# Optimization experiments

Hardware: AMD Instinct MI355X
Metric: run time of the kernel (lower is better)

Reference implementation:

```python
import jax, jax.numpy as jnp
import numpy as np

SNUM = 8           # number of select-PUF stages
PUF_LEN = 64       # arbiter PUF length -> phi dim = PUF_LEN + 1
BATCH = 262144     # number of challenge-response pairs
D = 2 ** SNUM      # 256 combinations


def _make_kron_tables():
    """Replicates the W/B kron construction from combineMPUF.__init__.
    Returns Wmat, Bmat of shape [SNUM, D]; row i is W[i]/B[i] (originally [1, D])."""
    tmpX = np.array([[1], [1]])
    Ws, Bs = [], []
    for i in range(SNUM):
        w = np.array([[-1], [1]])
        b = np.array([[1], [0]])
        for _ in range(i + 1, SNUM):
            w = np.kron(tmpX, w)
            b = np.kron(tmpX, b)
        for _ in range(i):
            w = np.kron(w, tmpX)
            b = np.kron(b, tmpX)
        Ws.append(w.T[0])
        Bs.append(b.T[0])
    return (jnp.asarray(np.stack(Ws), jnp.float32),
            jnp.asarray(np.stack(Bs), jnp.float32))


def setup_inputs() -> dict:
    key = jax.random.key(0)
    k_phi, k_ws, k_bs, k_wd, k_bd = jax.random.split(key, 5)
    F = PUF_LEN + 1
    scale = 1.0 / np.sqrt(F)  # ~ torch Linear init scale
    phi = jax.random.normal(k_phi, (BATCH, F), dtype=jnp.float32)
    W_S = jax.random.uniform(k_ws, (SNUM, F), jnp.float32, -scale, scale)
    b_S = jax.random.uniform(k_bs, (SNUM,), jnp.float32, -scale, scale)
    W_D = jax.random.uniform(k_wd, (D, F), jnp.float32, -scale, scale)
    b_D = jax.random.uniform(k_bd, (D,), jnp.float32, -scale, scale)
    Wmat, Bmat = _make_kron_tables()
    return {"phi": phi, "W_S": W_S, "b_S": b_S, "W_D": W_D, "b_D": b_D,
            "Wmat": Wmat, "Bmat": Bmat}


def reference(phi, W_S, b_S, W_D, b_D, Wmat, Bmat):
    # phi: [B, F]; W_S: [SNUM, F]; W_D: [D, F]; Wmat/Bmat: [SNUM, D]
    Sdelta = phi @ W_S.T + b_S            # [B, SNUM]
    Ddelta = phi @ W_D.T + b_D            # [B, D]
    Souts = jax.nn.sigmoid(Sdelta)        # [B, SNUM]
    Douts = jax.nn.sigmoid(Ddelta)        # [B, D]
    # sigmoid-gated outer-product chain: M = prod_i (s_i * w_i + b_i)
    M = jnp.ones_like(Douts)
    for i in range(SNUM):                 # small fixed structural loop
        M = M * (Souts[:, i:i + 1] * Wmat[i] + Bmat[i])
    ans = jnp.sum(Douts * M * 0.99999, axis=-1, keepdims=True)  # [B, 1]
    reliability_output = jnp.abs(Sdelta)  # [B, SNUM]
    return ans, reliability_output
```

## Files before the change

### kernel.cpp

```cpp
#include <hip/hip_runtime.h>

typedef float  f32x4  __attribute__((ext_vector_type(4)));
typedef float  f32x4a __attribute__((ext_vector_type(4), aligned(4)));
typedef float  f32x2a __attribute__((ext_vector_type(2), aligned(4)));
typedef __bf16 bf16x8 __attribute__((ext_vector_type(8)));
typedef short  short8 __attribute__((ext_vector_type(8)));

#define F      65
#define NTT    17
#define KS3    3
#define RPB    128

__device__ __forceinline__ float fast_sigmoid(float x) {
  float e = __builtin_amdgcn_exp2f(-1.4426950408889634f * x);
  return __builtin_amdgcn_rcpf(1.0f + e);
}
template<int CTRL>
__device__ __forceinline__ float dpp_mov(float v) {
  return __builtin_bit_cast(float,
    __builtin_amdgcn_update_dpp(0, __builtin_bit_cast(int, v), CTRL, 0xF, 0xF, true));
}
__device__ __forceinline__ float reduce16(float v) {
  v += dpp_mov<0xB1>(v);
  v += dpp_mov<0x4E>(v);
  v += dpp_mov<0x141>(v);
  v += dpp_mov<0x140>(v);
  return v;
}

__global__ void prep_w(const float* __restrict__ W_S, const float* __restrict__ b_S,
                       const float* __restrict__ W_D, const float* __restrict__ b_D,
                       unsigned short* __restrict__ wsb) {
  int b = blockIdx.x;
  int t = b / 3, s = b % 3;
  int l = threadIdx.x;
  int c = l & 15, q = l >> 4;
  short8 out;
#pragma unroll
  for (int j = 0; j < 8; ++j) {
    int k = 32 * s + 8 * q + j;
    float v = 0.0f;
    if (t < 16) {
      int n = 16 * t + c;
      if (k < F)       v = W_D[n * F + k];
      else if (k == F) v = b_D[n];
    } else if (c < 8) {
      if (k < F)       v = W_S[c * F + k];
      else if (k == F) v = b_S[c];
    }
    unsigned int u = __builtin_bit_cast(unsigned int, v);
    u += 0x7FFFu + ((u >> 16) & 1u);
    out[j] = (short)(u >> 16);
  }
  reinterpret_cast<short8*>(wsb)[b * 64 + l] = out;
}

__device__ __forceinline__ float ml_mt(float (*soutv)[9], float (*rowrec)[17],
                                       int R, int c) {
  f32x2a p01 = *reinterpret_cast<const f32x2a*>(&soutv[R][0]);
  f32x2a p23 = *reinterpret_cast<const f32x2a*>(&soutv[R][2]);
  f32x2a p45 = *reinterpret_cast<const f32x2a*>(&soutv[R][4]);
  f32x2a p67 = *reinterpret_cast<const f32x2a*>(&soutv[R][6]);
  float m = 0.99999f;
  m *= (c & 1) ? p01[0] : 1.0f - p01[0];
  m *= (c & 2) ? p01[1] : 1.0f - p01[1];
  m *= (c & 4) ? p23[0] : 1.0f - p23[0];
  m *= (c & 8) ? p23[1] : 1.0f - p23[1];
  float mt = (c & 1) ? p45[0] : 1.0f - p45[0];
  mt *= (c & 2) ? p45[1] : 1.0f - p45[1];
  mt *= (c & 4) ? p67[0] : 1.0f - p67[0];
  mt *= (c & 8) ? p67[1] : 1.0f - p67[1];
  rowrec[R][c] = mt;
  return m;
}

__launch_bounds__(256, 4)
__global__ void mpuf_main(const float* __restrict__ phi,
                          const unsigned short* __restrict__ wsb,
                          float* __restrict__ out_ans,
                          float* __restrict__ out_rel) {
  __shared__ float soutv[RPB][9];
  __shared__ float rowrec[RPB][17];

  const int tid  = threadIdx.x;
  const int wave = tid >> 6;
  const int l    = tid & 63;
  const int c    = l & 15;
  const int q    = l >> 4;
  const int wrow = wave * 32;
  const int brow = blockIdx.x * RPB;

  const float* prow0 = phi + (size_t)(brow + wrow + c) * F;
  const float* prow1 = prow0 + (size_t)16 * F;

  f32x4a f40[4], f41[4];
#pragma unroll
  for (int s = 0; s < 2; ++s) {
    f40[2 * s]     = *reinterpret_cast<const f32x4a*>(prow0 + 32 * s + 8 * q);
    f40[2 * s + 1] = *reinterpret_cast<const f32x4a*>(prow0 + 32 * s + 8 * q + 4);
    f41[2 * s]     = *reinterpret_cast<const f32x4a*>(prow1 + 32 * s + 8 * q);
    f41[2 * s + 1] = *reinterpret_cast<const f32x4a*>(prow1 + 32 * s + 8 * q + 4);
  }
  const float a640 = prow0[64];
  const float a641 = prow1[64];

  const short8* wsv = reinterpret_cast<const short8*>(wsb);
  short8 bS[3], bcur[6];
#pragma unroll
  for (int s = 0; s < 3; ++s) bS[s] = wsv[(16 * KS3 + s) * 64 + l];
#pragma unroll
  for (int i = 0; i < 6; ++i) bcur[i] = wsv[i * 64 + l];

  bf16x8 af0[3], af1[3];
#pragma unroll
  for (int s = 0; s < 2; ++s) {
    bf16x8 v0, v1;
#pragma unroll
    for (int j = 0; j < 4; ++j) {
      v0[j]     = (__bf16)f40[2 * s][j];
      v0[j + 4] = (__bf16)f40[2 * s + 1][j];
      v1[j]     = (__bf16)f41[2 * s][j];
      v1[j + 4] = (__bf16)f41[2 * s + 1][j];
    }
    af0[s] = v0; af1[s] = v1;
  }
  {
    bf16x8 v0 = {}, v1 = {};
    if (q == 0) {
      v0[0] = (__bf16)a640; v0[1] = (__bf16)1.0f;
      v1[0] = (__bf16)a641; v1[1] = (__bf16)1.0f;
    }
    af0[2] = v0; af1[2] = v1;
  }

  f32x4 aS0 = {}, aS1 = {};
#pragma unroll
  for (int s = 0; s < KS3; ++s) {
    bf16x8 b = __builtin_bit_cast(bf16x8, bS[s]);
    aS0 = __builtin_amdgcn_mfma_f32_16x16x32_bf16(af0[s], b, aS0, 0, 0, 0);
    aS1 = __builtin_amdgcn_mfma_f32_16x16x32_bf16(af1[s], b, aS1, 0, 0, 0);
  }
  if (c < 8) {
#pragma unroll
    for (int r = 0; r < 4; ++r) {
      const int R0 = wrow + q * 4 + r, R1 = R0 + 16;
      out_rel[(size_t)(brow + R0) * 8 + c] = fabsf(aS0[r]);
      out_rel[(size_t)(brow + R1) * 8 + c] = fabsf(aS1[r]);
      soutv[R0][c] = fast_sigmoid(aS0[r]);
      soutv[R1][c] = fast_sigmoid(aS1[r]);
    }
  }

  float Ml0[4], Ml1[4];
#pragma unroll
  for (int r = 0; r < 4; ++r) {
    const int R0 = wrow + q * 4 + r;
    Ml0[r] = ml_mt(soutv, rowrec, R0, c);
    Ml1[r] = ml_mt(soutv, rowrec, R0 + 16, c);
  }

  float ans0[4] = {0, 0, 0, 0}, ans1[4] = {0, 0, 0, 0};

#pragma unroll 1
  for (int tp = 0; tp < 8; ++tp) {
    f32x4 a00 = {}, a01 = {}, a10 = {}, a11 = {};
#pragma unroll
    for (int s = 0; s < KS3; ++s) {
      bf16x8 b0 = __builtin_bit_cast(bf16x8, bcur[s]);
      bf16x8 b1 = __builtin_bit_cast(bf16x8, bcur[3 + s]);
      a00 = __builtin_amdgcn_mfma_f32_16x16x32_bf16(af0[s], b0, a00, 0, 0, 0);
      a10 = __builtin_amdgcn_mfma_f32_16x16x32_bf16(af1[s], b0, a10, 0, 0, 0);
      a01 = __builtin_amdgcn_mfma_f32_16x16x32_bf16(af0[s], b1, a01, 0, 0, 0);
      a11 = __builtin_amdgcn_mfma_f32_16x16x32_bf16(af1[s], b1, a11, 0, 0, 0);
    }
    short8 bnxt[6];
    const int tpn = (tp < 7) ? tp + 1 : 7;
#pragma unroll
    for (int i = 0; i < 6; ++i) bnxt[i] = wsv[(tpn * 6 + i) * 64 + l];
#pragma unroll
    for (int r = 0; r < 4; ++r) {
      const int R0 = wrow + q * 4 + r, R1 = R0 + 16;
      f32x2a w0 = *reinterpret_cast<const f32x2a*>(&rowrec[R0][2 * tp]);
      f32x2a w1 = *reinterpret_cast<const f32x2a*>(&rowrec[R1][2 * tp]);
      ans0[r] = fmaf(fast_sigmoid(a00[r]), w0[0], ans0[r]);
      ans0[r] = fmaf(fast_sigmoid(a01[r]), w0[1], ans0[r]);
      ans1[r] = fmaf(fast_sigmoid(a10[r]), w1[0], ans1[r]);
      ans1[r] = fmaf(fast_sigmoid(a11[r]), w1[1], ans1[r]);
    }
#pragma unroll
    for (int i = 0; i < 6; ++i) bcur[i] = bnxt[i];
  }

#pragma unroll
  for (int r = 0; r < 4; ++r) {
    ans0[r] = reduce16(Ml0[r] * ans0[r]);
    ans1[r] = reduce16(Ml1[r] * ans1[r]);
  }
  if (c == 0) {
    f32x4 o0 = { ans0[0], ans0[1], ans0[2], ans0[3] };
    f32x4 o1 = { ans1[0], ans1[1], ans1[2], ans1[3] };
    *reinterpret_cast<f32x4*>(&out_ans[brow + wrow + q * 4])      = o0;
    *reinterpret_cast<f32x4*>(&out_ans[brow + wrow + 16 + q * 4]) = o1;
  }
}

extern "C" void kernel_launch(void* const* d_in, const int* in_sizes, int n_in,
                              void* d_out, int out_size, void* d_ws, size_t ws_size,
                              hipStream_t stream) {
  const float* phi = (const float*)d_in[0];
  const float* W_S = (const float*)d_in[1];
  const float* b_S = (const float*)d_in[2];
  const float* W_D = (const float*)d_in[3];
  const float* b_D = (const float*)d_in[4];
  const int rows = in_sizes[0] / F;
  unsigned short* wsb = (unsigned short*)d_ws;
  float* out_ans = (float*)d_out;
  float* out_rel = out_ans + rows;
  hipLaunchKernelGGL(prep_w, dim3(NTT * KS3), dim3(64), 0, stream,
                     W_S, b_S, W_D, b_D, wsb);
  hipLaunchKernelGGL(mpuf_main, dim3(rows / RPB), dim3(256), 0, stream,
                     phi, wsb, out_ans, out_rel);
}
```

Measured before the change: 43.23 us.

## Fold sigmoid scale into weights, halve per-iteration tiles, spill Ml to LDS

```diff
diff --git a/kernel.cpp b/kernel.cpp
--- a/kernel.cpp
+++ b/kernel.cpp
@@ -10,10 +10,14 @@
 #define NTT    17
 #define KS3    3
 #define RPB    128
+#define NEGL2E -1.4426950408889634f
 
 __device__ __forceinline__ float fast_sigmoid(float x) {
-  float e = __builtin_amdgcn_exp2f(-1.4426950408889634f * x);
+  float e = __builtin_amdgcn_exp2f(NEGL2E * x);
   return __builtin_amdgcn_rcpf(1.0f + e);
+}
+__device__ __forceinline__ float sig_prescaled(float a) {
+  return __builtin_amdgcn_rcpf(1.0f + __builtin_amdgcn_exp2f(a));
 }
 template<int CTRL>
 __device__ __forceinline__ float dpp_mov(float v) {
@@ -42,8 +46,8 @@
     float v = 0.0f;
     if (t < 16) {
       int n = 16 * t + c;
-      if (k < F)       v = W_D[n * F + k];
-      else if (k == F) v = b_D[n];
+      if (k < F)       v = NEGL2E * W_D[n * F + k];
+      else if (k == F) v = NEGL2E * b_D[n];
     } else if (c < 8) {
       if (k < F)       v = W_S[c * F + k];
       else if (k == F) v = b_S[c];
@@ -55,32 +59,14 @@
   reinterpret_cast<short8*>(wsb)[b * 64 + l] = out;
 }
 
-__device__ __forceinline__ float ml_mt(float (*soutv)[9], float (*rowrec)[17],
-                                       int R, int c) {
-  f32x2a p01 = *reinterpret_cast<const f32x2a*>(&soutv[R][0]);
-  f32x2a p23 = *reinterpret_cast<const f32x2a*>(&soutv[R][2]);
-  f32x2a p45 = *reinterpret_cast<const f32x2a*>(&soutv[R][4]);
-  f32x2a p67 = *reinterpret_cast<const f32x2a*>(&soutv[R][6]);
-  float m = 0.99999f;
-  m *= (c & 1) ? p01[0] : 1.0f - p01[0];
-  m *= (c & 2) ? p01[1] : 1.0f - p01[1];
-  m *= (c & 4) ? p23[0] : 1.0f - p23[0];
-  m *= (c & 8) ? p23[1] : 1.0f - p23[1];
-  float mt = (c & 1) ? p45[0] : 1.0f - p45[0];
-  mt *= (c & 2) ? p45[1] : 1.0f - p45[1];
-  mt *= (c & 4) ? p67[0] : 1.0f - p67[0];
-  mt *= (c & 8) ? p67[1] : 1.0f - p67[1];
-  rowrec[R][c] = mt;
-  return m;
-}
-
-__launch_bounds__(256, 4)
+__launch_bounds__(256, 5)
 __global__ void mpuf_main(const float* __restrict__ phi,
                           const unsigned short* __restrict__ wsb,
                           float* __restrict__ out_ans,
                           float* __restrict__ out_rel) {
   __shared__ float soutv[RPB][9];
-  __shared__ float rowrec[RPB][17];
+  __shared__ float mtrec[RPB][17];
+  __shared__ float mlrec[RPB][17];
 
   const int tid  = threadIdx.x;
   const int wave = tid >> 6;
@@ -105,11 +91,11 @@
   const float a641 = prow1[64];
 
   const short8* wsv = reinterpret_cast<const short8*>(wsb);
-  short8 bS[3], bcur[6];
-#pragma unroll
-  for (int s = 0; s < 3; ++s) bS[s] = wsv[(16 * KS3 + s) * 64 + l];
-#pragma unroll
-  for (int i = 0; i < 6; ++i) bcur[i] = wsv[i * 64 + l];
+  short8 bcur[3], bnxt[3];
+#pragma unroll
+  for (int s = 0; s < 3; ++s) bcur[s] = wsv[(16 * KS3 + s) * 64 + l];
+#pragma unroll
+  for (int s = 0; s < 3; ++s) bnxt[s] = wsv[s * 64 + l];
 
   bf16x8 af0[3], af1[3];
 #pragma unroll
@@ -136,7 +122,7 @@
   f32x4 aS0 = {}, aS1 = {};
 #pragma unroll
   for (int s = 0; s < KS3; ++s) {
-    bf16x8 b = __builtin_bit_cast(bf16x8, bS[s]);
+    bf16x8 b = __builtin_bit_cast(bf16x8, bcur[s]);
     aS0 = __builtin_amdgcn_mfma_f32_16x16x32_bf16(af0[s], b, aS0, 0, 0, 0);
     aS1 = __builtin_amdgcn_mfma_f32_16x16x32_bf16(af1[s], b, aS1, 0, 0, 0);
   }
@@ -151,50 +137,55 @@
     }
   }
 
-  float Ml0[4], Ml1[4];
-#pragma unroll
-  for (int r = 0; r < 4; ++r) {
-    const int R0 = wrow + q * 4 + r;
-    Ml0[r] = ml_mt(soutv, rowrec, R0, c);
-    Ml1[r] = ml_mt(soutv, rowrec, R0 + 16, c);
+#pragma unroll
+  for (int rr = 0; rr < 8; ++rr) {
+    const int R = wrow + (rr & 4) * 4 + q * 4 + (rr & 3);
+    f32x2a p01 = *reinterpret_cast<const f32x2a*>(&soutv[R][0]);
+    f32x2a p23 = *reinterpret_cast<const f32x2a*>(&soutv[R][2]);
+    f32x2a p45 = *reinterpret_cast<const f32x2a*>(&soutv[R][4]);
+    f32x2a p67 = *reinterpret_cast<const f32x2a*>(&soutv[R][6]);
+    float m = 0.99999f;
+    m *= (c & 1) ? p01[0] : 1.0f - p01[0];
+    m *= (c & 2) ? p01[1] : 1.0f - p01[1];
+    m *= (c & 4) ? p23[0] : 1.0f - p23[0];
+    m *= (c & 8) ? p23[1] : 1.0f - p23[1];
+    mlrec[R][c] = m;
+    float mt = (c & 1) ? p45[0] : 1.0f - p45[0];
+    mt *= (c & 2) ? p45[1] : 1.0f - p45[1];
+    mt *= (c & 4) ? p67[0] : 1.0f - p67[0];
+    mt *= (c & 8) ? p67[1] : 1.0f - p67[1];
+    mtrec[R][c] = mt;
   }
 
   float ans0[4] = {0, 0, 0, 0}, ans1[4] = {0, 0, 0, 0};
 
 #pragma unroll 1
-  for (int tp = 0; tp < 8; ++tp) {
-    f32x4 a00 = {}, a01 = {}, a10 = {}, a11 = {};
+  for (int t = 0; t < 16; ++t) {
+    f32x4 A0 = {}, A1 = {};
 #pragma unroll
     for (int s = 0; s < KS3; ++s) {
-      bf16x8 b0 = __builtin_bit_cast(bf16x8, bcur[s]);
-      bf16x8 b1 = __builtin_bit_cast(bf16x8, bcur[3 + s]);
-      a00 = __builtin_amdgcn_mfma_f32_16x16x32_bf16(af0[s], b0, a00, 0, 0, 0);
-      a10 = __builtin_amdgcn_mfma_f32_16x16x32_bf16(af1[s], b0, a10, 0, 0, 0);
-      a01 = __builtin_amdgcn_mfma_f32_16x16x32_bf16(af0[s], b1, a01, 0, 0, 0);
-      a11 = __builtin_amdgcn_mfma_f32_16x16x32_bf16(af1[s], b1, a11, 0, 0, 0);
-    }
-    short8 bnxt[6];
-    const int tpn = (tp < 7) ? tp + 1 : 7;
-#pragma unroll
-    for (int i = 0; i < 6; ++i) bnxt[i] = wsv[(tpn * 6 + i) * 64 + l];
+      bf16x8 b = __builtin_bit_cast(bf16x8, bnxt[s]);
+      A0 = __builtin_amdgcn_mfma_f32_16x16x32_bf16(af0[s], b, A0, 0, 0, 0);
+      A1 = __builtin_amdgcn_mfma_f32_16x16x32_bf16(af1[s], b, A1, 0, 0, 0);
+    }
+    const int tn = (t < 15) ? t + 1 : 15;
+#pragma unroll
+    for (int s = 0; s < 3; ++s) bnxt[s] = wsv[(tn * KS3 + s) * 64 + l];
 #pragma unroll
     for (int r = 0; r < 4; ++r) {
       const int R0 = wrow + q * 4 + r, R1 = R0 + 16;
-      f32x2a w0 = *reinterpret_cast<const f32x2a*>(&rowrec[R0][2 * tp]);
-      f32x2a w1 = *reinterpret_cast<const f32x2a*>(&rowrec[R1][2 * tp]);
-      ans0[r] = fmaf(fast_sigmoid(a00[r]), w0[0], ans0[r]);
-      ans0[r] = fmaf(fast_sigmoid(a01[r]), w0[1], ans0[r]);
-      ans1[r] = fmaf(fast_sigmoid(a10[r]), w1[0], ans1[r]);
-      ans1[r] = fmaf(fast_sigmoid(a11[r]), w1[1], ans1[r]);
-    }
-#pragma unroll
-    for (int i = 0; i < 6; ++i) bcur[i] = bnxt[i];
+      float w0 = mtrec[R0][t];
+      float w1 = mtrec[R1][t];
+      ans0[r] = fmaf(sig_prescaled(A0[r]), w0, ans0[r]);
+      ans1[r] = fmaf(sig_prescaled(A1[r]), w1, ans1[r]);
+    }
   }
 
 #pragma unroll
   for (int r = 0; r < 4; ++r) {
-    ans0[r] = reduce16(Ml0[r] * ans0[r]);
-    ans1[r] = reduce16(Ml1[r] * ans1[r]);
+    const int R0 = wrow + q * 4 + r, R1 = R0 + 16;
+    ans0[r] = reduce16(mlrec[R0][c] * ans0[r]);
+    ans1[r] = reduce16(mlrec[R1][c] * ans1[r]);
   }
   if (c == 0) {
     f32x4 o0 = { ans0[0], ans0[1], ans0[2], ans0[3] };
```

After: 41.24 us. -4.6%, faster.
